# Performance work log

Hardware: AMD Instinct MI355X
Metric: run time of the kernel (lower is better)

Reference implementation:

```python
import jax, jax.numpy as jnp
import numpy as np

N_NODES = 50000

def gcn_conv(x, W, b, src, dst, n):
    # PyG GCNConv: h = x @ W; add self-loops; sym-normalized mean aggregation; + bias
    h = x @ W  # [N, out]
    deg = jax.ops.segment_sum(jnp.ones(src.shape[0], x.dtype), dst, num_segments=n) + 1.0  # +1 self-loop
    dinv = jax.lax.rsqrt(deg)  # deg^{-1/2}
    norm = dinv[src] * dinv[dst]  # [E]
    msg = h[src] * norm[:, None]  # [E, out]
    agg = jax.ops.segment_sum(msg, dst, num_segments=n)
    agg = agg + h * (dinv * dinv)[:, None]  # self-loop contribution, norm = 1/deg
    return agg + b


def setup_inputs() -> dict:
    key = jax.random.key(0)
    ks = jax.random.split(key, 12)
    f1, h1, h2, a = 128, 128, 64, N_NODES
    def glorot(k, shape):
        lim = float(np.sqrt(6.0 / (shape[0] + shape[1])))
        return jax.random.uniform(k, shape, jnp.float32, -lim, lim)
    x = jax.random.normal(ks[0], (N_NODES, f1), jnp.float32)
    edge_index = jax.random.randint(ks[1], (2, 800000), 0, N_NODES, dtype=jnp.int64)
    W1 = glorot(ks[2], (f1, h1)); b1 = jnp.zeros((h1,), jnp.float32)
    W2 = glorot(ks[3], (h1, h2)); b2 = jnp.zeros((h2,), jnp.float32)
    W3 = glorot(ks[4], (h2, 1));  b3 = jnp.zeros((1,), jnp.float32)
    lim4 = float(1.0 / np.sqrt(a))
    W4 = jax.random.uniform(ks[5], (a,), jnp.float32, -lim4, lim4)
    b4 = jax.random.uniform(ks[6], (1,), jnp.float32, -lim4, lim4)
    return {"x": x, "edge_index": edge_index, "W1": W1, "b1": b1,
            "W2": W2, "b2": b2, "W3": W3, "b3": b3, "W4": W4, "b4": b4}


def reference(x, edge_index, W1, b1, W2, b2, W3, b3, W4, b4):
    src, dst = edge_index[0], edge_index[1]
    n = x.shape[0]
    h = jnp.tanh(gcn_conv(x, W1, b1, src, dst, n))
    h = jnp.tanh(gcn_conv(h, W2, b2, src, dst, n))
    h = jnp.tanh(gcn_conv(h, W3, b3, src, dst, n))
    h = h.reshape(-1)  # [N] == action_dim
    out = jnp.dot(W4, h) + b4  # Linear(action_dim, 1) -> [1]
    return out
```

## Files before the change

### kernel.cpp

```cpp
#include <hip/hip_runtime.h>
#include <math.h>


constexpr int BLOCK = 256;
constexpr int SLOTS = 64;

template<int K, int M>
__global__ void __launch_bounds__(256) gemm1_fill(const float* __restrict__ X,
                                                  const float* __restrict__ W,
                                                  float* __restrict__ H, int N, int ngemm,
                                                  const int* __restrict__ src,
                                                  const int* __restrict__ dst,
                                                  int* __restrict__ deg,
                                                  unsigned short* __restrict__ slots,
                                                  int E, int nfill) {
    __shared__ float xs[64][64];
    if (blockIdx.x % 3 == 2) {
        int blk = blockIdx.x / 3;
        if (blk >= nfill) return;
        int base = (blk * blockDim.x + threadIdx.x) * 8;
        if (base + 8 <= E) {
            int4 da = *reinterpret_cast<const int4*>(dst + base);
            int4 db = *reinterpret_cast<const int4*>(dst + base + 4);
            int4 sa = *reinterpret_cast<const int4*>(src + base);
            int4 sb = *reinterpret_cast<const int4*>(src + base + 4);
            int p0 = atomicAdd(&deg[da.x], 1);
            int p1 = atomicAdd(&deg[da.y], 1);
            int p2 = atomicAdd(&deg[da.z], 1);
            int p3 = atomicAdd(&deg[da.w], 1);
            int p4 = atomicAdd(&deg[db.x], 1);
            int p5 = atomicAdd(&deg[db.y], 1);
            int p6 = atomicAdd(&deg[db.z], 1);
            int p7 = atomicAdd(&deg[db.w], 1);
            if (p0 < SLOTS) slots[(size_t)da.x * SLOTS + p0] = (unsigned short)sa.x;
            if (p1 < SLOTS) slots[(size_t)da.y * SLOTS + p1] = (unsigned short)sa.y;
            if (p2 < SLOTS) slots[(size_t)da.z * SLOTS + p2] = (unsigned short)sa.z;
            if (p3 < SLOTS) slots[(size_t)da.w * SLOTS + p3] = (unsigned short)sa.w;
            if (p4 < SLOTS) slots[(size_t)db.x * SLOTS + p4] = (unsigned short)sb.x;
            if (p5 < SLOTS) slots[(size_t)db.y * SLOTS + p5] = (unsigned short)sb.y;
            if (p6 < SLOTS) slots[(size_t)db.z * SLOTS + p6] = (unsigned short)sb.z;
            if (p7 < SLOTS) slots[(size_t)db.w * SLOTS + p7] = (unsigned short)sb.w;
        } else {
            for (int e = base; e < E; ++e) {
                int d = dst[e];
                int p = atomicAdd(&deg[d], 1);
                if (p < SLOTS) slots[(size_t)d * SLOTS + p] = (unsigned short)src[e];
            }
        }
        return;
    }
    constexpr int BM = 64;
    constexpr int TN = 4;
    constexpr int TX = M / TN;
    constexpr int TY = 256 / TX;
    constexpr int TM = BM / TY;
    constexpr int KH4 = 16;

    int gblk = (blockIdx.x / 3) * 2 + (blockIdx.x % 3);
    if (gblk >= ngemm) return;
    const int tid = threadIdx.x;
    const int n0 = gblk * BM;

    const int tx = tid % TX;
    const int ty = tid / TX;
    const int col0 = tx * TN;
    const int row0 = ty * TM;

    float acc[TM][TN];
#pragma unroll
    for (int r = 0; r < TM; ++r)
#pragma unroll
        for (int c = 0; c < TN; ++c) acc[r][c] = 0.0f;

    const float4* X4 = reinterpret_cast<const float4*>(X);
    const float4* W4 = reinterpret_cast<const float4*>(W);
    constexpr int X4_PER_ROW = K / 4;
    constexpr int W4_PER_ROW = M / 4;

#pragma unroll
    for (int ph = 0; ph < 2; ++ph) {
#pragma unroll
        for (int i = 0; i < 4; ++i) {
            int idx = tid + i * 256;
            int row = idx >> 4;
            int k4 = idx & 15;
            float4 v = make_float4(0.f, 0.f, 0.f, 0.f);
            if (n0 + row < N) v = X4[(size_t)(n0 + row) * X4_PER_ROW + ph * KH4 + k4];
            *reinterpret_cast<float4*>(&xs[row][k4 * 4]) = v;
        }
        __syncthreads();
#pragma unroll 4
        for (int k4 = 0; k4 < KH4; ++k4) {
            int k4g = ph * KH4 + k4;
            float4 wv[4];
#pragma unroll
            for (int i = 0; i < 4; ++i)
                wv[i] = W4[(size_t)(k4g * 4 + i) * W4_PER_ROW + tx];
            float4 xv[TM];
#pragma unroll
            for (int r = 0; r < TM; ++r)
                xv[r] = *reinterpret_cast<const float4*>(&xs[row0 + r][k4 * 4]);
#pragma unroll
            for (int r = 0; r < TM; ++r) {
#pragma unroll
                for (int c = 0; c < TN; ++c) {
                    acc[r][c] = fmaf(xv[r].x, ((float*)&wv[0])[c], acc[r][c]);
                    acc[r][c] = fmaf(xv[r].y, ((float*)&wv[1])[c], acc[r][c]);
                    acc[r][c] = fmaf(xv[r].z, ((float*)&wv[2])[c], acc[r][c]);
                    acc[r][c] = fmaf(xv[r].w, ((float*)&wv[3])[c], acc[r][c]);
                }
            }
        }
        __syncthreads();
    }

#pragma unroll
    for (int r = 0; r < TM; ++r) {
        int row = n0 + row0 + r;
        if (row <= N) {
            float4 o;
            o.x = acc[r][0]; o.y = acc[r][1];
            o.z = acc[r][2]; o.w = acc[r][3];
            *reinterpret_cast<float4*>(&H[(size_t)row * M + col0]) = o;
        }
    }
}

__global__ void dinv_scale(const int* __restrict__ deg, float* __restrict__ dinv,
                           float4* __restrict__ H4, int N) {
    int idx = blockIdx.x * blockDim.x + threadIdx.x;
    int n = idx >> 5, q = idx & 31;
    if (n > N) return;
    if (n == N) { if (q == 0) dinv[N] = 0.0f; return; }
    float di = 1.0f / sqrtf((float)deg[n] + 1.0f);
    if (q == 0) dinv[n] = di;
    float4 v = H4[idx];
    v.x *= di; v.y *= di; v.z *= di; v.w *= di;
    H4[idx] = v;
}

template<int K, int M>
__global__ void __launch_bounds__(256) gemm_tiled(const float* __restrict__ X,
                                                  const float* __restrict__ W,
                                                  const float* __restrict__ dinv,
                                                  float* __restrict__ H, int N) {
    constexpr int BM = 64;
    constexpr int TN = 4;
    constexpr int TX = M / TN;
    constexpr int TY = 256 / TX;
    constexpr int TM = BM / TY;
    constexpr int K4 = K / 4;

    __shared__ float xs[BM][K];

    const int tid = threadIdx.x;
    const int n0 = blockIdx.x * BM;

    {
        const float4* X4 = reinterpret_cast<const float4*>(X);
        constexpr int F4_PER_ROW = K / 4;
        constexpr int TOT = BM * F4_PER_ROW;
#pragma unroll
        for (int i = 0; i < TOT / 256; ++i) {
            int idx = tid + i * 256;
            int row = idx / F4_PER_ROW;
            int k4 = idx % F4_PER_ROW;
            float4 v = make_float4(0.f, 0.f, 0.f, 0.f);
            if (n0 + row < N) v = X4[(size_t)(n0 + row) * F4_PER_ROW + k4];
            *reinterpret_cast<float4*>(&xs[row][k4 * 4]) = v;
        }
    }
    __syncthreads();

    const int tx = tid % TX;
    const int ty = tid / TX;
    const int col0 = tx * TN;
    const int row0 = ty * TM;

    float acc[TM][TN];
#pragma unroll
    for (int r = 0; r < TM; ++r)
#pragma unroll
        for (int c = 0; c < TN; ++c) acc[r][c] = 0.0f;

    const float4* W4 = reinterpret_cast<const float4*>(W);
    constexpr int W4_PER_ROW = M / 4;

#pragma unroll 4
    for (int k4 = 0; k4 < K4; ++k4) {
        float4 wv[4];
#pragma unroll
        for (int i = 0; i < 4; ++i)
            wv[i] = W4[(size_t)(k4 * 4 + i) * W4_PER_ROW + tx];
        float4 xv[TM];
#pragma unroll
        for (int r = 0; r < TM; ++r)
            xv[r] = *reinterpret_cast<const float4*>(&xs[row0 + r][k4 * 4]);
#pragma unroll
        for (int r = 0; r < TM; ++r) {
#pragma unroll
            for (int c = 0; c < TN; ++c) {
                acc[r][c] = fmaf(xv[r].x, ((float*)&wv[0])[c], acc[r][c]);
                acc[r][c] = fmaf(xv[r].y, ((float*)&wv[1])[c], acc[r][c]);
                acc[r][c] = fmaf(xv[r].z, ((float*)&wv[2])[c], acc[r][c]);
                acc[r][c] = fmaf(xv[r].w, ((float*)&wv[3])[c], acc[r][c]);
            }
        }
    }

#pragma unroll
    for (int r = 0; r < TM; ++r) {
        int row = n0 + row0 + r;
        if (row <= N) {
            float di = dinv[row];
            float4 o;
            o.x = acc[r][0] * di; o.y = acc[r][1] * di;
            o.z = acc[r][2] * di; o.w = acc[r][3] * di;
            *reinterpret_cast<float4*>(&H[(size_t)row * M + col0]) = o;
        }
    }
}

__global__ void __launch_bounds__(256) agg128(const int* __restrict__ deg,
                                              const unsigned short* __restrict__ slots,
                                              const float* __restrict__ Hs,
                                              const float* __restrict__ bias,
                                              float* __restrict__ A, int N) {
    int wid = threadIdx.x >> 6;
    int lane = threadIdx.x & 63;
    int n = blockIdx.x * 4 + wid;
    if (n >= N) return;
    int half = lane >> 5, sub = lane & 31;
    const float4* H4 = reinterpret_cast<const float4*>(Hs);
    float4 acc = make_float4(0.f, 0.f, 0.f, 0.f);
    if (half == 0) acc = H4[(size_t)n * 32 + sub];
    int dg = deg[n];
    int cnt = min(dg, SLOTS);
    int idxv = (lane < cnt) ? (int)slots[(size_t)n * SLOTS + lane] : N;
    int cnt16 = (cnt + 15) & ~15;
    for (int j = 0; j < cnt16; j += 16) {
        int s0 = __shfl(idxv, j + half);
        int s1 = __shfl(idxv, j + 2 + half);
        int s2 = __shfl(idxv, j + 4 + half);
        int s3 = __shfl(idxv, j + 6 + half);
        int s4 = __shfl(idxv, j + 8 + half);
        int s5 = __shfl(idxv, j + 10 + half);
        int s6 = __shfl(idxv, j + 12 + half);
        int s7 = __shfl(idxv, j + 14 + half);
        float4 v0 = H4[(size_t)s0 * 32 + sub];
        float4 v1 = H4[(size_t)s1 * 32 + sub];
        float4 v2 = H4[(size_t)s2 * 32 + sub];
        float4 v3 = H4[(size_t)s3 * 32 + sub];
        float4 v4 = H4[(size_t)s4 * 32 + sub];
        float4 v5 = H4[(size_t)s5 * 32 + sub];
        float4 v6 = H4[(size_t)s6 * 32 + sub];
        float4 v7 = H4[(size_t)s7 * 32 + sub];
        acc.x += (v0.x + v1.x) + (v2.x + v3.x) + (v4.x + v5.x) + (v6.x + v7.x);
        acc.y += (v0.y + v1.y) + (v2.y + v3.y) + (v4.y + v5.y) + (v6.y + v7.y);
        acc.z += (v0.z + v1.z) + (v2.z + v3.z) + (v4.z + v5.z) + (v6.z + v7.z);
        acc.w += (v0.w + v1.w) + (v2.w + v3.w) + (v4.w + v5.w) + (v6.w + v7.w);
    }
    acc.x += __shfl_down(acc.x, 32);
    acc.y += __shfl_down(acc.y, 32);
    acc.z += __shfl_down(acc.z, 32);
    acc.w += __shfl_down(acc.w, 32);
    if (half == 0) {
        float di = 1.0f / sqrtf((float)dg + 1.0f);
        float4 b = reinterpret_cast<const float4*>(bias)[sub];
        float4 o;
        o.x = tanhf(acc.x * di + b.x);
        o.y = tanhf(acc.y * di + b.y);
        o.z = tanhf(acc.z * di + b.z);
        o.w = tanhf(acc.w * di + b.w);
        reinterpret_cast<float4*>(A)[(size_t)n * 32 + sub] = o;
    }
}

__global__ void __launch_bounds__(256) agg64_dot3(const int* __restrict__ deg,
                                                  const unsigned short* __restrict__ slots,
                                                  const float* __restrict__ dinv,
                                                  const float* __restrict__ Hs,
                                                  const float* __restrict__ b2,
                                                  const float* __restrict__ W3,
                                                  float* __restrict__ Hs3, int N) {
    int wid = threadIdx.x >> 6;
    int lane = threadIdx.x & 63;
    int n = blockIdx.x * 4 + wid;
    if (n >= N) return;
    int grp = lane >> 4, sub = lane & 15;
    const float4* H4 = reinterpret_cast<const float4*>(Hs);
    float4 acc = make_float4(0.f, 0.f, 0.f, 0.f);
    if (grp == 0) acc = H4[(size_t)n * 16 + sub];
    int cnt = min(deg[n], SLOTS);
    int idxv = (lane < cnt) ? (int)slots[(size_t)n * SLOTS + lane] : N;
    int cnt16 = (cnt + 15) & ~15;
    int j = 0;
    for (; j + 32 <= cnt16; j += 32) {
        int s0 = __shfl(idxv, j + grp);
        int s1 = __shfl(idxv, j + 4 + grp);
        int s2 = __shfl(idxv, j + 8 + grp);
        int s3 = __shfl(idxv, j + 12 + grp);
        int s4 = __shfl(idxv, j + 16 + grp);
        int s5 = __shfl(idxv, j + 20 + grp);
        int s6 = __shfl(idxv, j + 24 + grp);
        int s7 = __shfl(idxv, j + 28 + grp);
        float4 v0 = H4[(size_t)s0 * 16 + sub];
        float4 v1 = H4[(size_t)s1 * 16 + sub];
        float4 v2 = H4[(size_t)s2 * 16 + sub];
        float4 v3 = H4[(size_t)s3 * 16 + sub];
        float4 v4 = H4[(size_t)s4 * 16 + sub];
        float4 v5 = H4[(size_t)s5 * 16 + sub];
        float4 v6 = H4[(size_t)s6 * 16 + sub];
        float4 v7 = H4[(size_t)s7 * 16 + sub];
        acc.x += (v0.x + v1.x) + (v2.x + v3.x) + (v4.x + v5.x) + (v6.x + v7.x);
        acc.y += (v0.y + v1.y) + (v2.y + v3.y) + (v4.y + v5.y) + (v6.y + v7.y);
        acc.z += (v0.z + v1.z) + (v2.z + v3.z) + (v4.z + v5.z) + (v6.z + v7.z);
        acc.w += (v0.w + v1.w) + (v2.w + v3.w) + (v4.w + v5.w) + (v6.w + v7.w);
    }
    for (; j < cnt16; j += 16) {
        int s0 = __shfl(idxv, j + grp);
        int s1 = __shfl(idxv, j + 4 + grp);
        int s2 = __shfl(idxv, j + 8 + grp);
        int s3 = __shfl(idxv, j + 12 + grp);
        float4 v0 = H4[(size_t)s0 * 16 + sub];
        float4 v1 = H4[(size_t)s1 * 16 + sub];
        float4 v2 = H4[(size_t)s2 * 16 + sub];
        float4 v3 = H4[(size_t)s3 * 16 + sub];
        acc.x += (v0.x + v1.x) + (v2.x + v3.x);
        acc.y += (v0.y + v1.y) + (v2.y + v3.y);
        acc.z += (v0.z + v1.z) + (v2.z + v3.z);
        acc.w += (v0.w + v1.w) + (v2.w + v3.w);
    }
    acc.x += __shfl_xor(acc.x, 16);
    acc.y += __shfl_xor(acc.y, 16);
    acc.z += __shfl_xor(acc.z, 16);
    acc.w += __shfl_xor(acc.w, 16);
    acc.x += __shfl_xor(acc.x, 32);
    acc.y += __shfl_xor(acc.y, 32);
    acc.z += __shfl_xor(acc.z, 32);
    acc.w += __shfl_xor(acc.w, 32);
    float di = dinv[n];
    float4 b = reinterpret_cast<const float4*>(b2)[sub];
    float4 w = reinterpret_cast<const float4*>(W3)[sub];
    float t = tanhf(acc.x * di + b.x) * w.x
            + tanhf(acc.y * di + b.y) * w.y
            + tanhf(acc.z * di + b.z) * w.z
            + tanhf(acc.w * di + b.w) * w.w;
#pragma unroll
    for (int off = 1; off < 16; off <<= 1) t += __shfl_xor(t, off);
    if (lane == 0) Hs3[n] = t * di;
}

__global__ void __launch_bounds__(256) agg_dot(const int* __restrict__ deg,
                                               const unsigned short* __restrict__ slots,
                                               const float* __restrict__ dinv,
                                               const float* __restrict__ Hs,
                                               const float* __restrict__ b3,
                                               const float* __restrict__ W4,
                                               float* __restrict__ partials, int N) {
    __shared__ float sm[4];
    int wid = threadIdx.x >> 6;
    int lane = threadIdx.x & 63;
    int n = blockIdx.x * 4 + wid;
    float p = 0.0f;
    if (n < N) {
        int cnt = min(deg[n], SLOTS);
        float acc = (lane < cnt) ? Hs[(int)slots[(size_t)n * SLOTS + lane]] : 0.0f;
#pragma unroll
        for (int off = 32; off > 0; off >>= 1) acc += __shfl_down(acc, off);
        if (lane == 0) {
            float h = tanhf((acc + Hs[n]) * dinv[n] + b3[0]);
            p = W4[n] * h;
        }
    }
    if (lane == 0) sm[wid] = p;
    __syncthreads();
    if (threadIdx.x == 0) partials[blockIdx.x] = sm[0] + sm[1] + sm[2] + sm[3];
}

__global__ void final_sum(const float* __restrict__ partials, int B,
                          const float* __restrict__ b4, float* __restrict__ out) {
    float acc = 0.0f;
    for (int i = threadIdx.x; i < B; i += blockDim.x) acc += partials[i];
#pragma unroll
    for (int off = 32; off > 0; off >>= 1) acc += __shfl_down(acc, off);
    __shared__ float sm[4];
    int lane = threadIdx.x & 63, wid = threadIdx.x >> 6;
    if (lane == 0) sm[wid] = acc;
    __syncthreads();
    if (threadIdx.x == 0) out[0] = sm[0] + sm[1] + sm[2] + sm[3] + b4[0];
}

extern "C" void kernel_launch(void* const* d_in, const int* in_sizes, int n_in,
                              void* d_out, int out_size, void* d_ws, size_t ws_size,
                              hipStream_t stream) {
    const float* x  = (const float*)d_in[0];
    const int*   ei = (const int*)d_in[1];
    const float* W1 = (const float*)d_in[2];
    const float* b1 = (const float*)d_in[3];
    const float* W2 = (const float*)d_in[4];
    const float* b2 = (const float*)d_in[5];
    const float* W3 = (const float*)d_in[6];
    const float* b3 = (const float*)d_in[7];
    const float* W4 = (const float*)d_in[8];
    const float* b4 = (const float*)d_in[9];

    const int N = in_sizes[0] / 128;
    const int E = in_sizes[1] / 2;
    const int* src = ei;
    const int* dst = ei + E;

    const int nblkW = (N + 3) / 4;

    float* base = (float*)d_ws;
    size_t off = 0;
    auto alloc = [&](size_t cnt, size_t align_f) -> float* {
        off = (off + align_f - 1) / align_f * align_f;
        float* p = base + off;
        off += cnt;
        return p;
    };
    int* deg     = (int*)alloc(N, 1);
    float* dinv  = alloc(N + 1, 1);
    unsigned short* slots = (unsigned short*)alloc((size_t)N * SLOTS / 2, 64);
    float* bufA  = alloc((size_t)(N + 1) * 128, 64);
    float* bufB  = alloc((size_t)(N + 1) * 128, 64);
    float* partials = alloc(nblkW, 64);

    float* hs2 = bufA;

    const int ngemm = (N + 63) / 64;
    const int nfill = (E + 2047) / 2048;
    const int ghalf = (ngemm + 1) / 2;
    const int nfused = 3 * ((ghalf > nfill) ? ghalf : nfill);
    const int nscale = (N * 32 + 32 + BLOCK - 1) / BLOCK;

    hipMemsetAsync(deg, 0, (size_t)N * sizeof(int), stream);
    gemm1_fill<128, 128><<<nfused, 256, 0, stream>>>(x, W1, bufA, N, ngemm,
                                                     src, dst, deg, slots, E, nfill);
    dinv_scale<<<nscale, BLOCK, 0, stream>>>(deg, dinv, (float4*)bufA, N);

    agg128<<<nblkW, 256, 0, stream>>>(deg, slots, bufA, b1, bufB, N);

    gemm_tiled<128, 64><<<ngemm, 256, 0, stream>>>(bufB, W2, dinv, hs2, N);
    agg64_dot3<<<nblkW, 256, 0, stream>>>(deg, slots, dinv, hs2, b2, W3, bufB, N);

    agg_dot<<<nblkW, 256, 0, stream>>>(deg, slots, dinv, bufB, b3, W4, partials, N);
    final_sum<<<1, BLOCK, 0, stream>>>(partials, nblkW, b4, (float*)d_out);
}
```

Baseline: 291.0 us.

## Fuse layer-2 GEMM into layer-1 aggregation via per-wave shuffle matvec

Drops the separate tiled GEMM for layer 2. Each wavefront now multiplies its aggregated, tanh-activated 128-wide row by W2 right away, using lane shuffles and W2 reads from global/L1, and writes the dinv-scaled 64-wide result. This avoids writing and re-reading the 128-wide intermediate activation and removes one kernel launch. The cost is that W2 is re-read for every node instead of reused from shared-memory tiles, and the agg kernel gets extra ALU and shuffle work.

```diff
diff --git a/kernel.cpp b/kernel.cpp
--- a/kernel.cpp
+++ b/kernel.cpp
@@ -139,97 +139,17 @@
     H4[idx] = v;
 }
 
-template<int K, int M>
-__global__ void __launch_bounds__(256) gemm_tiled(const float* __restrict__ X,
-                                                  const float* __restrict__ W,
-                                                  const float* __restrict__ dinv,
-                                                  float* __restrict__ H, int N) {
-    constexpr int BM = 64;
-    constexpr int TN = 4;
-    constexpr int TX = M / TN;
-    constexpr int TY = 256 / TX;
-    constexpr int TM = BM / TY;
-    constexpr int K4 = K / 4;
-
-    __shared__ float xs[BM][K];
-
-    const int tid = threadIdx.x;
-    const int n0 = blockIdx.x * BM;
-
-    {
-        const float4* X4 = reinterpret_cast<const float4*>(X);
-        constexpr int F4_PER_ROW = K / 4;
-        constexpr int TOT = BM * F4_PER_ROW;
-#pragma unroll
-        for (int i = 0; i < TOT / 256; ++i) {
-            int idx = tid + i * 256;
-            int row = idx / F4_PER_ROW;
-            int k4 = idx % F4_PER_ROW;
-            float4 v = make_float4(0.f, 0.f, 0.f, 0.f);
-            if (n0 + row < N) v = X4[(size_t)(n0 + row) * F4_PER_ROW + k4];
-            *reinterpret_cast<float4*>(&xs[row][k4 * 4]) = v;
-        }
-    }
-    __syncthreads();
-
-    const int tx = tid % TX;
-    const int ty = tid / TX;
-    const int col0 = tx * TN;
-    const int row0 = ty * TM;
-
-    float acc[TM][TN];
-#pragma unroll
-    for (int r = 0; r < TM; ++r)
-#pragma unroll
-        for (int c = 0; c < TN; ++c) acc[r][c] = 0.0f;
-
-    const float4* W4 = reinterpret_cast<const float4*>(W);
-    constexpr int W4_PER_ROW = M / 4;
-
-#pragma unroll 4
-    for (int k4 = 0; k4 < K4; ++k4) {
-        float4 wv[4];
-#pragma unroll
-        for (int i = 0; i < 4; ++i)
-            wv[i] = W4[(size_t)(k4 * 4 + i) * W4_PER_ROW + tx];
-        float4 xv[TM];
-#pragma unroll
-        for (int r = 0; r < TM; ++r)
-            xv[r] = *reinterpret_cast<const float4*>(&xs[row0 + r][k4 * 4]);
-#pragma unroll
-        for (int r = 0; r < TM; ++r) {
-#pragma unroll
-            for (int c = 0; c < TN; ++c) {
-                acc[r][c] = fmaf(xv[r].x, ((float*)&wv[0])[c], acc[r][c]);
-                acc[r][c] = fmaf(xv[r].y, ((float*)&wv[1])[c], acc[r][c]);
-                acc[r][c] = fmaf(xv[r].z, ((float*)&wv[2])[c], acc[r][c]);
-                acc[r][c] = fmaf(xv[r].w, ((float*)&wv[3])[c], acc[r][c]);
-            }
-        }
-    }
-
-#pragma unroll
-    for (int r = 0; r < TM; ++r) {
-        int row = n0 + row0 + r;
-        if (row <= N) {
-            float di = dinv[row];
-            float4 o;
-            o.x = acc[r][0] * di; o.y = acc[r][1] * di;
-            o.z = acc[r][2] * di; o.w = acc[r][3] * di;
-            *reinterpret_cast<float4*>(&H[(size_t)row * M + col0]) = o;
-        }
-    }
-}
-
-__global__ void __launch_bounds__(256) agg128(const int* __restrict__ deg,
-                                              const unsigned short* __restrict__ slots,
-                                              const float* __restrict__ Hs,
-                                              const float* __restrict__ bias,
-                                              float* __restrict__ A, int N) {
+__global__ void __launch_bounds__(256) agg128_g2(const int* __restrict__ deg,
+                                                 const unsigned short* __restrict__ slots,
+                                                 const float* __restrict__ Hs,
+                                                 const float* __restrict__ b1,
+                                                 const float* __restrict__ W2,
+                                                 float* __restrict__ hs2, int N) {
     int wid = threadIdx.x >> 6;
     int lane = threadIdx.x & 63;
     int n = blockIdx.x * 4 + wid;
-    if (n >= N) return;
+    if (n > N) return;
+    if (n == N) { hs2[(size_t)N * 64 + lane] = 0.0f; return; }
     int half = lane >> 5, sub = lane & 31;
     const float4* H4 = reinterpret_cast<const float4*>(Hs);
     float4 acc = make_float4(0.f, 0.f, 0.f, 0.f);
@@ -264,16 +184,29 @@
     acc.y += __shfl_down(acc.y, 32);
     acc.z += __shfl_down(acc.z, 32);
     acc.w += __shfl_down(acc.w, 32);
-    if (half == 0) {
-        float di = 1.0f / sqrtf((float)dg + 1.0f);
-        float4 b = reinterpret_cast<const float4*>(bias)[sub];
-        float4 o;
-        o.x = tanhf(acc.x * di + b.x);
-        o.y = tanhf(acc.y * di + b.y);
-        o.z = tanhf(acc.z * di + b.z);
-        o.w = tanhf(acc.w * di + b.w);
-        reinterpret_cast<float4*>(A)[(size_t)n * 32 + sub] = o;
-    }
+    float din = 1.0f / sqrtf((float)dg + 1.0f);
+    float4 t;
+    {
+        float4 b = reinterpret_cast<const float4*>(b1)[sub];
+        t.x = tanhf(acc.x * din + b.x);
+        t.y = tanhf(acc.y * din + b.y);
+        t.z = tanhf(acc.z * din + b.z);
+        t.w = tanhf(acc.w * din + b.w);
+    }
+    float om = 0.0f;
+#pragma unroll 8
+    for (int ks = 0; ks < 32; ++ks) {
+        float a0 = __shfl(t.x, ks);
+        float a1 = __shfl(t.y, ks);
+        float a2 = __shfl(t.z, ks);
+        float a3 = __shfl(t.w, ks);
+        int k = ks * 4;
+        om = fmaf(a0, W2[(k + 0) * 64 + lane], om);
+        om = fmaf(a1, W2[(k + 1) * 64 + lane], om);
+        om = fmaf(a2, W2[(k + 2) * 64 + lane], om);
+        om = fmaf(a3, W2[(k + 3) * 64 + lane], om);
+    }
+    hs2[(size_t)n * 64 + lane] = om * din;
 }
 
 __global__ void __launch_bounds__(256) agg64_dot3(const int* __restrict__ deg,
@@ -427,7 +360,8 @@
     float* bufB  = alloc((size_t)(N + 1) * 128, 64);
     float* partials = alloc(nblkW, 64);
 
-    float* hs2 = bufA;
+    float* hs2 = bufB;
+    float* hs3 = bufB + (size_t)(N + 1) * 64;
 
     const int ngemm = (N + 63) / 64;
     const int nfill = (E + 2047) / 2048;
@@ -440,11 +374,10 @@
                                                      src, dst, deg, slots, E, nfill);
     dinv_scale<<<nscale, BLOCK, 0, stream>>>(deg, dinv, (float4*)bufA, N);
 
-    agg128<<<nblkW, 256, 0, stream>>>(deg, slots, bufA, b1, bufB, N);
-
-    gemm_tiled<128, 64><<<ngemm, 256, 0, stream>>>(bufB, W2, dinv, hs2, N);
-    agg64_dot3<<<nblkW, 256, 0, stream>>>(deg, slots, dinv, hs2, b2, W3, bufB, N);
-
-    agg_dot<<<nblkW, 256, 0, stream>>>(deg, slots, dinv, bufB, b3, W4, partials, N);
+    agg128_g2<<<nblkW + 1, 256, 0, stream>>>(deg, slots, bufA, b1, W2, hs2, N);
+
+    agg64_dot3<<<nblkW, 256, 0, stream>>>(deg, slots, dinv, hs2, b2, W3, hs3, N);
+
+    agg_dot<<<nblkW, 256, 0, stream>>>(deg, slots, dinv, hs3, b3, W4, partials, N);
     final_sum<<<1, BLOCK, 0, stream>>>(partials, nblkW, b4, (float*)d_out);
 }
```

Result: no change. 295.2 us (+1.5%).
